# Kernel tuning notes

Hardware: AMD Instinct MI355X
Metric: run time of the kernel (lower is better)

The kernel has to match this reference:

```python
import jax, jax.numpy as jnp
import numpy as np

P, N, GRID, C, S, STEPS, N_ADJ = 128, 512, 112, 64, 128, 3, 4
HW = GRID * GRID
IN_DIM = C + 2


def _ring_adjacency():
    # prepare_gcn_component builds a ring graph: each vertex connected to
    # n_adj nearest neighbors along the polygon, row-normalized.
    offs = np.concatenate([np.arange(1, N_ADJ // 2 + 1), -np.arange(1, N_ADJ // 2 + 1)])
    A = np.zeros((N, N), np.float32)
    idx = np.arange(N)
    for o in offs:
        A[idx, (idx + o) % N] = 1.0
    A /= A.sum(1, keepdims=True)
    return jnp.asarray(A)


def setup_inputs() -> dict:
    key = jax.random.key(0)
    ks = jax.random.split(key, 10)
    std = 0.01  # matches m.weight.data.normal_(0.0, 0.01)
    return {
        "feature": jax.random.normal(ks[0], (P, HW, C), jnp.float32),
        "init_polys": jax.random.uniform(ks[1], (P, N, 2), jnp.float32),
        "adj": _ring_adjacency(),
        "W1s": jax.random.normal(ks[2], (STEPS, IN_DIM, S), jnp.float32) * std,
        "W1n": jax.random.normal(ks[3], (STEPS, IN_DIM, S), jnp.float32) * std,
        "b1": jnp.zeros((STEPS, S), jnp.float32),
        "W2s": jax.random.normal(ks[4], (STEPS, S, S), jnp.float32) * std,
        "W2n": jax.random.normal(ks[5], (STEPS, S, S), jnp.float32) * std,
        "b2": jnp.zeros((STEPS, S), jnp.float32),
        "Wfc": jax.random.normal(ks[6], (STEPS, S, 2), jnp.float32) * std,
        "bfc": jnp.zeros((STEPS, 2), jnp.float32),
    }


def _gather(feat, ids):
    # feat: [P, HW, C], ids: [P, N] int -> [P, N, C]
    return jnp.take_along_axis(feat, ids[:, :, None], axis=1)


def _nearest_sample(feature, poly):
    # step-0 `sampling` path: gather at floor(coord*grid) flat indices
    X0 = jnp.clip(jnp.floor(poly[..., 0] * GRID), 0, GRID - 1)
    Y0 = jnp.clip(jnp.floor(poly[..., 1] * GRID), 0, GRID - 1)
    ids = (X0 + Y0 * GRID).astype(jnp.int32)
    return _gather(feature, ids)


def _interpolated_sum(feature, poly):
    Xs = poly[..., 0] * GRID
    Ys = poly[..., 1] * GRID
    X0 = jnp.floor(Xs); X1 = X0 + 1.0
    Y0 = jnp.floor(Ys); Y1 = Y0 + 1.0
    w00 = (X1 - Xs) * (Y1 - Ys)
    w01 = (X1 - Xs) * (Ys - Y0)
    w10 = (Xs - X0) * (Y1 - Ys)
    w11 = (Xs - X0) * (Ys - Y0)
    X0c = jnp.clip(X0, 0, GRID - 1).astype(jnp.int32)
    X1c = jnp.clip(X1, 0, GRID - 1).astype(jnp.int32)
    Y0c = jnp.clip(Y0, 0, GRID - 1).astype(jnp.int32)
    Y1c = jnp.clip(Y1, 0, GRID - 1).astype(jnp.int32)
    M00 = _gather(feature, X0c + Y0c * GRID)
    M01 = _gather(feature, X0c + Y1c * GRID)
    M10 = _gather(feature, X1c + Y0c * GRID)
    M11 = _gather(feature, X1c + Y1c * GRID)
    return (w00[..., None] * M00 + w01[..., None] * M01 +
            w10[..., None] * M10 + w11[..., None] * M11)


def _gconv(x, adj, Ws, Wn, b):
    # x: [P, N, D]; adj: [N, N] (shared ring graph)
    nbr = jnp.einsum('nm,pmd->pnd', adj, x)
    return x @ Ws + nbr @ Wn + b


def _gcn(x, adj, i, W1s, W1n, b1, W2s, W2n, b2, Wfc, bfc):
    h = jax.nn.relu(_gconv(x, adj, W1s[i], W1n[i], b1[i]))
    h = jax.nn.relu(_gconv(h, adj, W2s[i], W2n[i], b2[i]))
    return h @ Wfc[i] + bfc[i]  # [P, N, 2]


def reference(feature, init_polys, adj, W1s, W1n, b1, W2s, W2n, b2, Wfc, bfc):
    poly = init_polys
    for i in range(STEPS):
        cnn_feat = _nearest_sample(feature, poly) if i == 0 else _interpolated_sum(feature, poly)
        inp = jnp.concatenate([cnn_feat, poly], axis=2)  # [P, N, C+2]
        pred = _gcn(inp, adj, i, W1s, W1n, b1, W2s, W2n, b2, Wfc, bfc)
        poly = poly + pred
    return poly
```

## Files before the change

### kernel.cpp

```cpp
#include <hip/hip_runtime.h>

#define P_      128
#define NV      512
#define GRID_   112
#define HW_     (GRID_*GRID_)
#define C_      64
#define S_      128

typedef short bf16x8 __attribute__((ext_vector_type(8)));
typedef float f32x4  __attribute__((ext_vector_type(4)));

__device__ __forceinline__ unsigned short f2bf(float x) {
    union { float f; unsigned int u; } v; v.f = x;
    unsigned int r = (v.u + 0x7FFFu + ((v.u >> 16) & 1u)) >> 16;
    return (unsigned short)r;
}
__device__ __forceinline__ float2 up2(unsigned int u) {
    union { unsigned int u; float f; } a, b;
    a.u = u << 16; b.u = u & 0xFFFF0000u;
    return make_float2(a.f, b.f);
}
__device__ __forceinline__ unsigned int pk2(float lo, float hi) {
    return (unsigned int)f2bf(lo) | ((unsigned int)f2bf(hi) << 16);
}

__global__ __launch_bounds__(256) void wprep_kernel(
    const float* __restrict__ W1s, const float* __restrict__ W1n,
    const float* __restrict__ W2s, const float* __restrict__ W2n,
    unsigned short* __restrict__ W1p, unsigned short* __restrict__ W2p)
{
    int idx = blockIdx.x * 256 + threadIdx.x;
    const int N1 = 3 * 5 * 8 * 64 * 8;
    const int N2 = 3 * 8 * 8 * 64 * 8;
    if (idx < N1) {
        int j = idx & 7, lane = (idx >> 3) & 63, nt = (idx >> 9) & 7;
        int ks = (idx >> 12) % 5, step = idx / 20480;
        int n = nt * 16 + (lane & 15);
        int k = ks * 32 + (lane >> 4) * 8 + j;
        float v = 0.f;
        if (k < 66)       v = W1s[(step * 66 + k) * 128 + n];
        else if (k < 132) v = W1n[(step * 66 + (k - 66)) * 128 + n];
        W1p[idx] = f2bf(v);
    } else if (idx < N1 + N2) {
        int e = idx - N1;
        int j = e & 7, lane = (e >> 3) & 63, nt = (e >> 9) & 7;
        int ks = (e >> 12) & 7, step = e >> 15;
        int n = nt * 16 + (lane & 15);
        int k = ks * 32 + (lane >> 4) * 8 + j;
        float v = (k < 128) ? W2s[(step * 128 + k) * 128 + n]
                            : W2n[(step * 128 + (k - 128)) * 128 + n];
        W2p[e] = f2bf(v);
    }
}

__global__ __launch_bounds__(256) void sample_kernel(
    const float* __restrict__ feature, const float* __restrict__ poly,
    unsigned short* __restrict__ inp, int nearest)
{
    int w = threadIdx.x >> 6, lane = threadIdx.x & 63;
    int g = blockIdx.x * 4 + w;
    int p = g >> 9;
    float px = poly[2 * g], py = poly[2 * g + 1];
    const float* fb = feature + (size_t)p * HW_ * C_;
    float val;
    if (nearest) {
        float X0 = fminf(fmaxf(floorf(px * (float)GRID_), 0.f), (float)(GRID_ - 1));
        float Y0 = fminf(fmaxf(floorf(py * (float)GRID_), 0.f), (float)(GRID_ - 1));
        int id = (int)X0 + (int)Y0 * GRID_;
        val = fb[(size_t)id * C_ + lane];
    } else {
        float Xs = px * (float)GRID_, Ys = py * (float)GRID_;
        float X0 = floorf(Xs), Y0 = floorf(Ys);
        float X1 = X0 + 1.f, Y1 = Y0 + 1.f;
        float ax = X1 - Xs, bx = Xs - X0;
        float ay = Y1 - Ys, by = Ys - Y0;
        int X0c = (int)fminf(fmaxf(X0, 0.f), (float)(GRID_ - 1));
        int X1c = (int)fminf(fmaxf(X1, 0.f), (float)(GRID_ - 1));
        int Y0c = (int)fminf(fmaxf(Y0, 0.f), (float)(GRID_ - 1));
        int Y1c = (int)fminf(fmaxf(Y1, 0.f), (float)(GRID_ - 1));
        float m00 = fb[(size_t)(X0c + Y0c * GRID_) * C_ + lane];
        float m01 = fb[(size_t)(X0c + Y1c * GRID_) * C_ + lane];
        float m10 = fb[(size_t)(X1c + Y0c * GRID_) * C_ + lane];
        float m11 = fb[(size_t)(X1c + Y1c * GRID_) * C_ + lane];
        val = (ax * ay) * m00 + (ax * by) * m01 + (bx * ay) * m10 + (bx * by) * m11;
    }
    unsigned short* row = inp + (size_t)g * 72;
    row[lane] = f2bf(val);
    if (lane < 8)
        row[64 + lane] = (lane == 0) ? f2bf(px) : (lane == 1) ? f2bf(py) : 0;
}

__global__ __launch_bounds__(256, 4) void gcn_kernel(
    const unsigned short* __restrict__ inp,
    const unsigned short* __restrict__ W1p,
    const float* __restrict__ b1,
    const unsigned short* __restrict__ W2p,
    const float* __restrict__ b2,
    const float* __restrict__ Wfc, const float* __restrict__ bfc,
    const float* __restrict__ poly_in, float* __restrict__ poly_out)
{
    __shared__ __align__(16) char smem[38016];
    unsigned int*   raw_u = (unsigned int*)smem;
    unsigned int*   A1_u  = (unsigned int*)(smem + 10368);
    unsigned short* h1s   = (unsigned short*)smem;
    unsigned int*   R2_u  = (unsigned int*)(smem + 21120);
    float*          h2    = (float*)smem;

    int p = blockIdx.x >> 3, n0 = (blockIdx.x & 7) * 64;
    int wv = threadIdx.x >> 6, lane = threadIdx.x & 63;
    int m = lane & 15, q = lane >> 4;
    int nt0 = wv * 2;

    const uint4* inp4 = (const uint4*)(inp + (size_t)p * NV * 72);
    uint4* raw4 = (uint4*)smem;
    for (int idx = threadIdx.x; idx < 72 * 9; idx += 256) {
        int r = idx / 9, u = idx - r * 9;
        raw4[idx] = inp4[(size_t)((n0 + r - 4) & 511) * 9 + u];
    }
    __syncthreads();

    for (int idx = threadIdx.x; idx < 80 * 84; idx += 256) {
        int a = idx / 84, u = idx - a * 84;
        unsigned int val = 0u;
        if (a < 68) {
            if (u < 33) {
                val = raw_u[(a + 2) * 36 + u];
            } else if (u < 66) {
                int uu = u - 33;
                float2 fa = up2(raw_u[a * 36 + uu]),       fb2 = up2(raw_u[(a + 1) * 36 + uu]);
                float2 fc = up2(raw_u[(a + 3) * 36 + uu]), fd  = up2(raw_u[(a + 4) * 36 + uu]);
                val = pk2(0.25f * (fa.x + fb2.x + fc.x + fd.x),
                          0.25f * (fa.y + fb2.y + fc.y + fd.y));
            }
        }
        A1_u[idx] = val;
    }
    __syncthreads();

    f32x4 acc1[5][2];
    #pragma unroll
    for (int i = 0; i < 5; i++) {
        acc1[i][0] = (f32x4){0.f, 0.f, 0.f, 0.f};
        acc1[i][1] = (f32x4){0.f, 0.f, 0.f, 0.f};
    }
    const bf16x8* B1 = (const bf16x8*)W1p;
    const unsigned short* A1s = (const unsigned short*)A1_u;
    #pragma unroll
    for (int ks = 0; ks < 5; ks++) {
        bf16x8 bfr0 = B1[(ks * 8 + nt0) * 64 + lane];
        bf16x8 bfr1 = B1[(ks * 8 + nt0 + 1) * 64 + lane];
        #pragma unroll
        for (int mt = 0; mt < 5; mt++) {
            bf16x8 a = *(const bf16x8*)(A1s + (mt * 16 + m) * 168 + ks * 32 + q * 8);
            acc1[mt][0] = __builtin_amdgcn_mfma_f32_16x16x32_bf16(a, bfr0, acc1[mt][0], 0, 0, 0);
            acc1[mt][1] = __builtin_amdgcn_mfma_f32_16x16x32_bf16(a, bfr1, acc1[mt][1], 0, 0, 0);
        }
    }
    __syncthreads();

    #pragma unroll
    for (int mt = 0; mt < 5; mt++) {
        #pragma unroll
        for (int j = 0; j < 2; j++) {
            int col = (nt0 + j) * 16 + m;
            float bias = b1[col];
            #pragma unroll
            for (int rg = 0; rg < 4; rg++) {
                int row = mt * 16 + q * 4 + rg;
                h1s[row * 132 + col] = f2bf(fmaxf(acc1[mt][j][rg] + bias, 0.f));
            }
        }
    }
    __syncthreads();

    const unsigned int* h1u = (const unsigned int*)h1s;
    for (int idx = threadIdx.x; idx < 64 * 64; idx += 256) {
        int a = idx >> 6, u = idx & 63;
        float2 fa = up2(h1u[a * 66 + u]),       fb2 = up2(h1u[(a + 1) * 66 + u]);
        float2 fc = up2(h1u[(a + 3) * 66 + u]), fd  = up2(h1u[(a + 4) * 66 + u]);
        R2_u[a * 66 + u] = pk2(0.25f * (fa.x + fb2.x + fc.x + fd.x),
                               0.25f * (fa.y + fb2.y + fc.y + fd.y));
    }
    __syncthreads();

    f32x4 acc2[4][2];
    #pragma unroll
    for (int i = 0; i < 4; i++) {
        acc2[i][0] = (f32x4){0.f, 0.f, 0.f, 0.f};
        acc2[i][1] = (f32x4){0.f, 0.f, 0.f, 0.f};
    }
    const bf16x8* B2 = (const bf16x8*)W2p;
    const unsigned short* selfS = h1s + 2 * 132;
    const unsigned short* ringS = (const unsigned short*)R2_u;
    #pragma unroll
    for (int ks = 0; ks < 8; ks++) {
        bf16x8 bfr0 = B2[(ks * 8 + nt0) * 64 + lane];
        bf16x8 bfr1 = B2[(ks * 8 + nt0 + 1) * 64 + lane];
        #pragma unroll
        for (int mt = 0; mt < 4; mt++) {
            const unsigned short* ap = (ks < 4)
                ? selfS + (mt * 16 + m) * 132 + ks * 32 + q * 8
                : ringS + (mt * 16 + m) * 132 + (ks - 4) * 32 + q * 8;
            bf16x8 a = *(const bf16x8*)ap;
            acc2[mt][0] = __builtin_amdgcn_mfma_f32_16x16x32_bf16(a, bfr0, acc2[mt][0], 0, 0, 0);
            acc2[mt][1] = __builtin_amdgcn_mfma_f32_16x16x32_bf16(a, bfr1, acc2[mt][1], 0, 0, 0);
        }
    }
    __syncthreads();

    #pragma unroll
    for (int mt = 0; mt < 4; mt++) {
        #pragma unroll
        for (int j = 0; j < 2; j++) {
            int col = (nt0 + j) * 16 + m;
            float bias = b2[col];
            #pragma unroll
            for (int rg = 0; rg < 4; rg++) {
                int row = mt * 16 + q * 4 + rg;
                h2[row * 129 + col] = fmaxf(acc2[mt][j][rg] + bias, 0.f);
            }
        }
    }
    __syncthreads();

    {
        int t = threadIdx.x;
        int oi = t >> 1, half = t & 1;
        int v = oi >> 1, j = oi & 1;
        const float* hv = h2 + v * 129 + half * 64;
        const float* wf = Wfc + half * 128 + j;
        float s0 = 0.f, s1 = 0.f, s2 = 0.f, s3 = 0.f;
        #pragma unroll
        for (int cc = 0; cc < 64; cc += 4) {
            s0 += hv[cc]     * wf[2 * cc];
            s1 += hv[cc + 1] * wf[2 * cc + 2];
            s2 += hv[cc + 2] * wf[2 * cc + 4];
            s3 += hv[cc + 3] * wf[2 * cc + 6];
        }
        float pr = (s0 + s1) + (s2 + s3) + (half ? 0.f : bfc[j]);
        pr += __shfl_xor(pr, 1);
        if (half == 0) {
            size_t o = ((size_t)p * NV + n0 + v) * 2 + j;
            poly_out[o] = poly_in[o] + pr;
        }
    }
}

extern "C" void kernel_launch(void* const* d_in, const int* in_sizes, int n_in,
                              void* d_out, int out_size, void* d_ws, size_t ws_size,
                              hipStream_t stream)
{
    const float* feature    = (const float*)d_in[0];
    const float* init_polys = (const float*)d_in[1];
    const float* W1s = (const float*)d_in[3];
    const float* W1n = (const float*)d_in[4];
    const float* b1  = (const float*)d_in[5];
    const float* W2s = (const float*)d_in[6];
    const float* W2n = (const float*)d_in[7];
    const float* b2  = (const float*)d_in[8];
    const float* Wfc = (const float*)d_in[9];
    const float* bfc = (const float*)d_in[10];
    float* out = (float*)d_out;

    char* wsb = (char*)d_ws;
    float* polyA = (float*)wsb;                  wsb += (size_t)P_ * NV * 2 * 4;
    float* polyB = (float*)wsb;                  wsb += (size_t)P_ * NV * 2 * 4;
    unsigned short* W1p = (unsigned short*)wsb;  wsb += (size_t)61440 * 2;
    unsigned short* W2p = (unsigned short*)wsb;  wsb += (size_t)98304 * 2;
    unsigned short* inp = (unsigned short*)wsb;

    wprep_kernel<<<624, 256, 0, stream>>>(W1s, W1n, W2s, W2n, W1p, W2p);

    const float* pin = init_polys;
    for (int i = 0; i < 3; i++) {
        float* pout = (i == 2) ? out : ((i == 0) ? polyA : polyB);
        sample_kernel<<<P_ * NV / 4, 256, 0, stream>>>(feature, pin, inp, i == 0);
        gcn_kernel<<<P_ * 8, 256, 0, stream>>>(
            inp, W1p + (size_t)i * 20480, b1 + i * 128,
            W2p + (size_t)i * 32768, b2 + i * 128,
            Wfc + i * 256, bfc + i * 2,
            pin, pout);
        pin = pout;
    }
}
```

Measured before the change: 623.3 us.

## Fuse feature sampling into GCN kernel, removing intermediate bf16 input buffer

Removes the separate sample_kernel and performs nearest and bilinear feature gathering directly inside gcn_kernel. Each block stages the polygon coordinates for its 64 vertices plus the 4-vertex halo on each side into shared memory, gathers features into the raw bf16 shared buffer, and pads the coordinate columns. This drops one launch per step and the global write and read of the intermediate input array. In exchange, the halo vertices (72 rows for 64 outputs) are sampled redundantly by neighbouring blocks, and the GCN blocks now carry gather latency themselves.

Measured after the change: 600.9 us. 3.6% less time.

```diff
diff --git a/kernel.cpp b/kernel.cpp
--- a/kernel.cpp
+++ b/kernel.cpp
@@ -53,69 +53,76 @@
     }
 }
 
-__global__ __launch_bounds__(256) void sample_kernel(
-    const float* __restrict__ feature, const float* __restrict__ poly,
-    unsigned short* __restrict__ inp, int nearest)
-{
-    int w = threadIdx.x >> 6, lane = threadIdx.x & 63;
-    int g = blockIdx.x * 4 + w;
-    int p = g >> 9;
-    float px = poly[2 * g], py = poly[2 * g + 1];
-    const float* fb = feature + (size_t)p * HW_ * C_;
-    float val;
-    if (nearest) {
-        float X0 = fminf(fmaxf(floorf(px * (float)GRID_), 0.f), (float)(GRID_ - 1));
-        float Y0 = fminf(fmaxf(floorf(py * (float)GRID_), 0.f), (float)(GRID_ - 1));
-        int id = (int)X0 + (int)Y0 * GRID_;
-        val = fb[(size_t)id * C_ + lane];
-    } else {
-        float Xs = px * (float)GRID_, Ys = py * (float)GRID_;
-        float X0 = floorf(Xs), Y0 = floorf(Ys);
-        float X1 = X0 + 1.f, Y1 = Y0 + 1.f;
-        float ax = X1 - Xs, bx = Xs - X0;
-        float ay = Y1 - Ys, by = Ys - Y0;
-        int X0c = (int)fminf(fmaxf(X0, 0.f), (float)(GRID_ - 1));
-        int X1c = (int)fminf(fmaxf(X1, 0.f), (float)(GRID_ - 1));
-        int Y0c = (int)fminf(fmaxf(Y0, 0.f), (float)(GRID_ - 1));
-        int Y1c = (int)fminf(fmaxf(Y1, 0.f), (float)(GRID_ - 1));
-        float m00 = fb[(size_t)(X0c + Y0c * GRID_) * C_ + lane];
-        float m01 = fb[(size_t)(X0c + Y1c * GRID_) * C_ + lane];
-        float m10 = fb[(size_t)(X1c + Y0c * GRID_) * C_ + lane];
-        float m11 = fb[(size_t)(X1c + Y1c * GRID_) * C_ + lane];
-        val = (ax * ay) * m00 + (ax * by) * m01 + (bx * ay) * m10 + (bx * by) * m11;
-    }
-    unsigned short* row = inp + (size_t)g * 72;
-    row[lane] = f2bf(val);
-    if (lane < 8)
-        row[64 + lane] = (lane == 0) ? f2bf(px) : (lane == 1) ? f2bf(py) : 0;
-}
-
 __global__ __launch_bounds__(256, 4) void gcn_kernel(
-    const unsigned short* __restrict__ inp,
+    const float* __restrict__ feature,
     const unsigned short* __restrict__ W1p,
     const float* __restrict__ b1,
     const unsigned short* __restrict__ W2p,
     const float* __restrict__ b2,
     const float* __restrict__ Wfc, const float* __restrict__ bfc,
-    const float* __restrict__ poly_in, float* __restrict__ poly_out)
+    const float* __restrict__ poly_in, float* __restrict__ poly_out,
+    int nearest)
 {
     __shared__ __align__(16) char smem[38016];
+    unsigned short* rawS  = (unsigned short*)smem;
     unsigned int*   raw_u = (unsigned int*)smem;
     unsigned int*   A1_u  = (unsigned int*)(smem + 10368);
     unsigned short* h1s   = (unsigned short*)smem;
     unsigned int*   R2_u  = (unsigned int*)(smem + 21120);
     float*          h2    = (float*)smem;
+    float2*         polyS = (float2*)(smem + 36864);
 
     int p = blockIdx.x >> 3, n0 = (blockIdx.x & 7) * 64;
     int wv = threadIdx.x >> 6, lane = threadIdx.x & 63;
     int m = lane & 15, q = lane >> 4;
     int nt0 = wv * 2;
 
-    const uint4* inp4 = (const uint4*)(inp + (size_t)p * NV * 72);
-    uint4* raw4 = (uint4*)smem;
-    for (int idx = threadIdx.x; idx < 72 * 9; idx += 256) {
-        int r = idx / 9, u = idx - r * 9;
-        raw4[idx] = inp4[(size_t)((n0 + r - 4) & 511) * 9 + u];
+    const float* fb    = feature + (size_t)p * HW_ * C_;
+    const float* pbase = poly_in + (size_t)p * NV * 2;
+
+    if (threadIdx.x < 72) {
+        int vtx = (n0 + (int)threadIdx.x - 4) & (NV - 1);
+        polyS[threadIdx.x] = ((const float2*)pbase)[vtx];
+    }
+    __syncthreads();
+
+    #pragma unroll 6
+    for (int i = 0; i < 18; i++) {
+        int u = i * 256 + threadIdx.x;
+        int r = u >> 6, ch = u & 63;
+        float2 pp = polyS[r];
+        float val;
+        if (nearest) {
+            float X0 = fminf(fmaxf(floorf(pp.x * (float)GRID_), 0.f), (float)(GRID_ - 1));
+            float Y0 = fminf(fmaxf(floorf(pp.y * (float)GRID_), 0.f), (float)(GRID_ - 1));
+            int id = (int)X0 + (int)Y0 * GRID_;
+            val = fb[(size_t)id * C_ + ch];
+        } else {
+            float Xs = pp.x * (float)GRID_, Ys = pp.y * (float)GRID_;
+            float X0 = floorf(Xs), Y0 = floorf(Ys);
+            float X1 = X0 + 1.f, Y1 = Y0 + 1.f;
+            float ax = X1 - Xs, bx = Xs - X0;
+            float ay = Y1 - Ys, by = Ys - Y0;
+            int X0c = (int)fminf(fmaxf(X0, 0.f), (float)(GRID_ - 1));
+            int X1c = (int)fminf(fmaxf(X1, 0.f), (float)(GRID_ - 1));
+            int Y0c = (int)fminf(fmaxf(Y0, 0.f), (float)(GRID_ - 1));
+            int Y1c = (int)fminf(fmaxf(Y1, 0.f), (float)(GRID_ - 1));
+            float m00 = fb[(size_t)(X0c + Y0c * GRID_) * C_ + ch];
+            float m01 = fb[(size_t)(X0c + Y1c * GRID_) * C_ + ch];
+            float m10 = fb[(size_t)(X1c + Y0c * GRID_) * C_ + ch];
+            float m11 = fb[(size_t)(X1c + Y1c * GRID_) * C_ + ch];
+            val = (ax * ay) * m00 + (ax * by) * m01 + (bx * ay) * m10 + (bx * by) * m11;
+        }
+        rawS[r * 72 + ch] = f2bf(val);
+    }
+    if (threadIdx.x < 72) {
+        float2 pp = polyS[threadIdx.x];
+        unsigned short* row = rawS + threadIdx.x * 72;
+        row[64] = f2bf(pp.x);
+        row[65] = f2bf(pp.y);
+        ((unsigned int*)row)[33] = 0u;
+        ((unsigned int*)row)[34] = 0u;
+        ((unsigned int*)row)[35] = 0u;
     }
     __syncthreads();
 
@@ -266,20 +273,19 @@
     float* polyA = (float*)wsb;                  wsb += (size_t)P_ * NV * 2 * 4;
     float* polyB = (float*)wsb;                  wsb += (size_t)P_ * NV * 2 * 4;
     unsigned short* W1p = (unsigned short*)wsb;  wsb += (size_t)61440 * 2;
-    unsigned short* W2p = (unsigned short*)wsb;  wsb += (size_t)98304 * 2;
-    unsigned short* inp = (unsigned short*)wsb;
+    unsigned short* W2p = (unsigned short*)wsb;
 
     wprep_kernel<<<624, 256, 0, stream>>>(W1s, W1n, W2s, W2n, W1p, W2p);
 
     const float* pin = init_polys;
     for (int i = 0; i < 3; i++) {
         float* pout = (i == 2) ? out : ((i == 0) ? polyA : polyB);
-        sample_kernel<<<P_ * NV / 4, 256, 0, stream>>>(feature, pin, inp, i == 0);
         gcn_kernel<<<P_ * 8, 256, 0, stream>>>(
-            inp, W1p + (size_t)i * 20480, b1 + i * 128,
+            feature,
+            W1p + (size_t)i * 20480, b1 + i * 128,
             W2p + (size_t)i * 32768, b2 + i * 128,
             Wfc + i * 256, bfc + i * 2,
-            pin, pout);
+            pin, pout, i == 0);
         pin = pout;
     }
 }
```
